# Kernel tuning notes

Hardware: AMD Instinct MI355X
Metric: run time of the kernel (lower is better)

The kernel has to match this reference:

```python
import jax, jax.numpy as jnp
import numpy as np

MIN_MAP = jnp.array([-3.602826, -3.602826, -3.602826], dtype=jnp.float32)

def _conv(x, w, stride, pad):
    return jax.lax.conv_general_dilated(x, w, (stride, stride), [(pad, pad), (pad, pad)],
                                        dimension_numbers=('NCHW', 'OIHW', 'NCHW'))

def _bn(x, g, b):
    # inference BatchNorm with running_mean=0, running_var=1 -> pure channel affine
    return x * g[None, :, None, None] + b[None, :, None, None]

def _maxpool2(x):
    return jax.lax.reduce_window(x, -jnp.inf, jax.lax.max, (1, 1, 2, 2), (1, 1, 2, 2), 'VALID')

def _rotations(angles):
    # angles: [N,3] (already multiplied by pi); matrix entries copied verbatim from the torch source
    c, s = jnp.cos(angles), jnp.sin(angles)
    z = jnp.zeros_like(c[:, 0]); o = jnp.ones_like(c[:, 0])
    Rx = jnp.stack([jnp.stack([o, z, z], -1),
                    jnp.stack([z, c[:, 0], s[:, 0]], -1),
                    jnp.stack([z, -s[:, 0], c[:, 0]], -1)], 1)
    Ry = jnp.stack([jnp.stack([c[:, 1], z, -s[:, 1]], -1),
                    jnp.stack([z, o, z], -1),
                    jnp.stack([s[:, 1], z, c[:, 1]], -1)], 1)
    Rz = jnp.stack([jnp.stack([c[:, 2], s[:, 2], z], -1),
                    jnp.stack([-s[:, 2], c[:, 2], z], -1),
                    jnp.stack([z, z, o], -1)], 1)
    return jnp.einsum('nij,njk,nkl->nil', Rx, Ry, Rz)  # [N,3,3]


def setup_inputs() -> dict:
    key = jax.random.key(0)
    ks = jax.random.split(key, 16)
    N, C, T, V, M = 32, 3, 224, 224, 2
    OC = 128
    def he(k, shape, fan_in):
        return jax.random.normal(k, shape, jnp.float32) * np.float32(np.sqrt(2.0 / fan_in))
    inp = {}
    inp['x'] = jax.random.normal(ks[0], (N, C, T, V, M), jnp.float32)
    inp['w1'] = he(ks[1], (OC, C, 5, 5), C * 25); inp['b1'] = jnp.zeros((OC,), jnp.float32)
    inp['g1'] = jnp.ones((OC,), jnp.float32); inp['be1'] = jnp.zeros((OC,), jnp.float32)
    inp['w2'] = he(ks[2], (OC, OC, 5, 5), OC * 25); inp['b2'] = jnp.zeros((OC,), jnp.float32)
    inp['g2'] = jnp.ones((OC,), jnp.float32); inp['be2'] = jnp.zeros((OC,), jnp.float32)
    feat = OC * (224 // 8) * (224 // 8)  # 100352
    inp['fw'] = jax.random.normal(ks[3], (6, feat), jnp.float32) * np.float32(np.sqrt(1.0 / feat))
    inp['fb'] = jnp.zeros((6,), jnp.float32)
    chans = [3, 64, 256, 512, 1024, 2048]  # surrogate ResNet-50-style /32 backbone
    for i in range(5):
        cin, cout = chans[i], chans[i + 1]
        inp['bw%d' % (i + 1)] = he(ks[4 + i], (cout, cin, 3, 3), cin * 9)
        inp['bg%d' % (i + 1)] = jnp.ones((cout,), jnp.float32)
        inp['bb%d' % (i + 1)] = jnp.zeros((cout,), jnp.float32)
    lin = 2048 * 7 * 7
    inp['lw'] = jax.random.normal(ks[10], (60, lin), jnp.float32) * np.float32(np.sqrt(1.0 / lin))
    inp['lb'] = jnp.zeros((60,), jnp.float32)
    return inp


def reference(x, w1, b1, g1, be1, w2, b2, g2, be2, fw, fb,
              bw1, bg1, bb1, bw2, bg2, bb2, bw3, bg3, bb3, bw4, bg4, bb4, bw5, bg5, bb5,
              lw, lb):
    N = x.shape[0]
    def person(xp):  # xp: [N,3,T,V]
        h = jax.nn.relu(_bn(_conv(xp, w1, 2, 2) + b1[None, :, None, None], g1, be1))
        h = jax.nn.relu(_bn(_conv(h, w2, 2, 2) + b2[None, :, None, None], g2, be2))
        h = _maxpool2(h)                       # [N,128,28,28]
        o = h.reshape(N, -1) @ fw.T + fb       # [N,6]
        # torch builds rotations from out[n,:3].item() -> constants w.r.t. autodiff
        R = _rotations(jax.lax.stop_gradient(o[:, :3]) * jnp.pi)
        xf = xp.reshape(N, 3, -1)
        rot = jnp.einsum('nij,njk->nik', R, xf)
        shift = jnp.einsum('nij,nj->ni', R, MIN_MAP[None, :] - o[:, 3:])
        bias = 255.0 * (shift - MIN_MAP[None, :]) / 8.812765
        z = (rot + bias[:, :, None]).reshape(xp.shape)
        for w, g, b in ((bw1, bg1, bb1), (bw2, bg2, bb2), (bw3, bg3, bb3),
                        (bw4, bg4, bb4), (bw5, bg5, bb5)):
            z = jax.nn.relu(_bn(_conv(z, w, 2, 1), g, b))
        return z  # [N,2048,7,7]
    out = jnp.maximum(person(x[..., 0]), person(x[..., 1]))
    return out.reshape(N, -1) @ lw.T + lb  # [N,60]
```

## Files before the change

kernel.cpp:

```cpp
#include <hip/hip_runtime.h>
#include <hip/hip_bf16.h>

typedef unsigned short u16;
typedef __attribute__((ext_vector_type(8))) short bf16x8;
typedef __attribute__((ext_vector_type(4))) float f32x4;
typedef __attribute__((ext_vector_type(8))) unsigned short u16x8;
typedef __attribute__((ext_vector_type(4))) unsigned short u16x4;

__device__ __forceinline__ u16 f2bf(float v) {
    __hip_bfloat16 b = __float2bfloat16(v);
    return *reinterpret_cast<u16*>(&b);
}
__device__ __forceinline__ float bf2f(u16 u) {
    __hip_bfloat16 b;
    *reinterpret_cast<u16*>(&b) = u;
    return __bfloat162float(b);
}

__device__ __forceinline__ void gl_lds16(const u16* g, u16* l) {
    __builtin_amdgcn_global_load_lds(
        (const __attribute__((address_space(1))) void*)g,
        (__attribute__((address_space(3))) void*)l, 16, 0, 0);
}

__global__ void repack_w32(const float* __restrict__ w, u16* __restrict__ wh,
                           int Cout, int Cin, int KK) {
    int i = blockIdx.x * blockDim.x + threadIdx.x;
    int tot = Cout * Cin * KK;
    if (i >= tot) return;
    int oc = i / (Cin * KK);
    int r = i - oc * (Cin * KK);
    int p = r / Cin, ic = r - p * Cin;
    wh[(size_t)oc * (Cin * KK) + (size_t)p * Cin + ic] =
        f2bf(w[((size_t)oc * Cin + ic) * KK + p]);
}
__global__ void repack_split2(const float* __restrict__ w, u16* __restrict__ Ap,
                              int Cout, int CinR, int CinP, int KK, int Ksteps) {
    int cols = Ksteps * 64;
    int idx = blockIdx.x * blockDim.x + threadIdx.x;
    int tot = Cout * cols;
    if (idx >= tot) return;
    int oc = idx / cols, c = idx - oc * cols;
    int t = c >> 6, r = c & 63, half = r >> 5, j = r & 31;
    int kk = t * 32 + j;
    int p = kk / CinP, ic = kk - p * CinP;
    float v = (p < KK && ic < CinR) ? w[((size_t)oc * CinR + ic) * KK + p] : 0.f;
    u16 h = f2bf(v);
    Ap[idx] = half ? f2bf(v - bf2f(h)) : h;
}
__global__ void repack_g4_2(const float* __restrict__ w, u16* __restrict__ Ap,
                            int Cout, int CinR, int KS, int Ksteps) {
    int cols = Ksteps * 64;
    int idx = blockIdx.x * blockDim.x + threadIdx.x;
    int tot = Cout * cols;
    if (idx >= tot) return;
    int oc = idx / cols, c = idx - oc * cols;
    int t = c >> 6, r = c & 63, half = r >> 5, j = r & 31;
    int pix = j >> 2, ch = j & 3;
    float v = (pix < KS && ch < CinR)
                  ? w[(((size_t)oc * CinR + ch) * KS + t) * KS + pix] : 0.f;
    u16 h = f2bf(v);
    Ap[idx] = half ? f2bf(v - bf2f(h)) : h;
}
__global__ void repack_g4(const float* __restrict__ w, u16* __restrict__ Ap,
                          int Cout, int CinR, int KS, int Kpp) {
    int idx = blockIdx.x * blockDim.x + threadIdx.x;
    int tot = Cout * Kpp;
    if (idx >= tot) return;
    int oc = idx / Kpp, kk = idx - oc * Kpp;
    int ky = kk >> 5, r = kk & 31;
    int pix = r >> 2, ch = r & 3;
    float v = (pix < KS && ch < CinR)
                  ? w[(((size_t)oc * CinR + ch) * KS + ky) * KS + pix] : 0.f;
    Ap[idx] = f2bf(v);
}

__global__ void extract_person4(const float* __restrict__ x,
                                u16* __restrict__ X4, int m, int total) {
    int idx = blockIdx.x * blockDim.x + threadIdx.x;
    if (idx >= total) return;
    int n = idx / 50176;
    int p = idx - n * 50176;
    int y = p / 224, xx = p - y * 224;
    u16 h[4];
    h[3] = 0;
#pragma unroll
    for (int c = 0; c < 3; ++c)
        h[c] = f2bf(x[(((size_t)(n * 3 + c)) * 50176 + p) * 2 + m]);
    size_t o = (((size_t)n * 228 + y + 2) * 232 + xx + 2) * 4;
    *reinterpret_cast<u16x4*>(&X4[o]) = *reinterpret_cast<u16x4*>(h);
}

__global__ void zero_u16(u16* __restrict__ b, size_t n8) {
    size_t i = (size_t)blockIdx.x * blockDim.x + threadIdx.x;
    if (i >= n8) return;
    u16x8 z = {0, 0, 0, 0, 0, 0, 0, 0};
    *reinterpret_cast<u16x8*>(&b[i * 8]) = z;
}
__global__ void zero_halo(u16* __restrict__ buf, int Nn, int Hp, int Wp, int C,
                          int P, int H, int W) {
    int idx = blockIdx.x * blockDim.x + threadIdx.x;
    int tot = Nn * Hp * Wp;
    if (idx >= tot) return;
    int x = idx % Wp, t = idx / Wp, y = t % Hp;
    if (y >= P && y < P + H && x >= P && x < P + W) return;
    u16* p = buf + (size_t)idx * C;
    u16x8 z = {0, 0, 0, 0, 0, 0, 0, 0};
    for (int c = 0; c < C; c += 8) *reinterpret_cast<u16x8*>(&p[c]) = z;
}

template <int BM, int CT, bool SPLIT, int MOUT>
__global__ __launch_bounds__(256) void gconv(
    const u16* __restrict__ A, const u16* __restrict__ B,
    const float* __restrict__ cbias, const float* __restrict__ gam,
    const float* __restrict__ bet,
    u16* __restrict__ outp, float* __restrict__ outf,
    int Nblk, int NHW, int Ksteps, int KSP,
    int Cin, int Hp_i, int Wp_i, int KS,
    int Wout, int HWout,
    int Cout, int Hp_o, int Wp_o, int P_o) {
    constexpr int WAVES_M = (BM == 128) ? 2 : 1;
    constexpr int WM = BM / WAVES_M;
    constexpr int WN = 128 / (4 / WAVES_M);
    constexpr int FM = WM / 16, FN = WN / 16;
    constexpr int ACOLS = SPLIT ? 64 : 32;
    constexpr int AR = (BM * ACOLS * 2) / 4096;

    __shared__ __align__(16) u16 Asb[2][BM * ACOLS];
    __shared__ __align__(16) u16 Bsb[2][128 * 32];

    const int tid = threadIdx.x;
    const int lane = tid & 63, wv = tid >> 6;

    const int nwg = gridDim.x, orig = blockIdx.x;
    const int qq = nwg >> 3, rr = nwg & 7, xcd = orig & 7;
    const int L = (xcd < rr ? xcd * (qq + 1) : rr * (qq + 1) + (xcd - rr) * qq) + (orig >> 3);
    const int gmK = nwg / Nblk;
    const int gm = gmK / KSP;
    const int bn = L / gmK;
    const int midK = L - bn * gmK;
    const int bm = midK % gm;
    const int kc = midK / gm;
    const int s0 = bn * 128, oc0 = bm * BM;

    const int nsteps = Ksteps;
    const int Arow = Ksteps * ACOLS;

    const u16* asrc[AR];
#pragma unroll
    for (int r = 0; r < AR; ++r) {
        int idx = r * 256 + tid;
        if constexpr (SPLIT) {
            int row = idx >> 3, slot = idx & 7;
            int c = slot ^ (row & 7);
            asrc[r] = A + (size_t)(oc0 + row) * Arow + c * 8;
        } else {
            int row = idx >> 2, slot = idx & 3;
            int q = slot ^ ((row >> 1) & 3);
            asrc[r] = A + (size_t)(oc0 + row) * Arow + q * 8;
        }
    }
    long brow[2];
#pragma unroll
    for (int r = 0; r < 2; ++r) {
        int idx = r * 256 + tid;
        int srow = idx >> 2;
        int q = (idx & 3) ^ ((idx >> 3) & 3);
        int s = s0 + srow;
        if (s > NHW - 1) s = NHW - 1;
        int n = s / HWout, pos = s - n * HWout;
        int oy = pos / Wout, ox = pos - oy * Wout;
        brow[r] = (((long)n * Hp_i + 2 * oy) * Wp_i + 2 * ox) * Cin + q * 8;
    }

    auto stage = [&](int buf, int t) {
        long ao = (long)t * ACOLS;
#pragma unroll
        for (int r = 0; r < AR; ++r)
            gl_lds16(asrc[r] + ao, &Asb[buf][(r * 256 + wv * 64) * 8]);
        long so;
        if constexpr (CT == 32) {
            int csn = Cin >> 5;
            int p = t / csn, cs = t - p * csn;
            int ky = p / KS, kx = p - ky * KS;
            so = (long)(ky * Wp_i + kx) * Cin + cs * 32;
        } else {
            so = (long)t * Wp_i * 4;
        }
#pragma unroll
        for (int r = 0; r < 2; ++r)
            gl_lds16(B + brow[r] + so, &Bsb[buf][(r * 256 + wv * 64) * 8]);
    };

    const int cl = lane & 15, oct = lane >> 4;
    const int octx = oct ^ ((cl >> 1) & 3);
    const int aslot = oct ^ (cl & 7);
    const int wm0 = (WAVES_M == 2) ? (wv & 1) * WM : 0;
    const int wn0 = (WAVES_M == 2) ? (wv >> 1) * WN : wv * WN;

    f32x4 acc[FM][FN] = {};

    const int cs_steps = nsteps / KSP;
    const int t0 = kc * cs_steps, t1 = t0 + cs_steps;

    stage(0, t0);
    __syncthreads();
    for (int t = t0; t < t1; ++t) {
        const int cur = (t - t0) & 1;
        if (t + 1 < t1) stage(cur ^ 1, t + 1);
        bf16x8 af[FM], bfr[FN];
#pragma unroll
        for (int mi = 0; mi < FM; ++mi) {
            if constexpr (SPLIT)
                af[mi] = *reinterpret_cast<const bf16x8*>(
                    &Asb[cur][(wm0 + mi * 16 + cl) * ACOLS + aslot * 8]);
            else
                af[mi] = *reinterpret_cast<const bf16x8*>(
                    &Asb[cur][(wm0 + mi * 16 + cl) * ACOLS + octx * 8]);
        }
#pragma unroll
        for (int ni = 0; ni < FN; ++ni)
            bfr[ni] = *reinterpret_cast<const bf16x8*>(
                &Bsb[cur][(wn0 + ni * 16 + cl) * 32 + octx * 8]);
#pragma unroll
        for (int mi = 0; mi < FM; ++mi)
#pragma unroll
            for (int ni = 0; ni < FN; ++ni)
                acc[mi][ni] = __builtin_amdgcn_mfma_f32_16x16x32_bf16(
                    af[mi], bfr[ni], acc[mi][ni], 0, 0, 0);
        if constexpr (SPLIT) {
            bf16x8 al[FM];
#pragma unroll
            for (int mi = 0; mi < FM; ++mi)
                al[mi] = *reinterpret_cast<const bf16x8*>(
                    &Asb[cur][(wm0 + mi * 16 + cl) * ACOLS + (aslot ^ 4) * 8]);
#pragma unroll
            for (int mi = 0; mi < FM; ++mi)
#pragma unroll
                for (int ni = 0; ni < FN; ++ni)
                    acc[mi][ni] = __builtin_amdgcn_mfma_f32_16x16x32_bf16(
                        al[mi], bfr[ni], acc[mi][ni], 0, 0, 0);
        }
        __syncthreads();
    }

#pragma unroll
    for (int ni = 0; ni < FN; ++ni) {
        int s = s0 + wn0 + ni * 16 + cl;
        if (s >= NHW) continue;
        int n = s / HWout, pos = s - n * HWout;
        int oy = pos / Wout, ox = pos - oy * Wout;
#pragma unroll
        for (int mi = 0; mi < FM; ++mi) {
            int oc = oc0 + wm0 + mi * 16 + oct * 4;
            if constexpr (MOUT == 3) {
                float* pf = outf + (size_t)kc * ((size_t)NHW * Cout);
#pragma unroll
                for (int r3 = 0; r3 < 4; ++r3)
                    pf[((size_t)n * Cout + oc + r3) * HWout + pos] = acc[mi][ni][r3];
            } else if constexpr (MOUT == 2) {
#pragma unroll
                for (int r3 = 0; r3 < 4; ++r3) {
                    float v = acc[mi][ni][r3];
                    if (cbias) v += cbias[oc + r3];
                    v = fmaf(v, gam[oc + r3], bet[oc + r3]);
                    v = fmaxf(v, 0.f);
                    outf[((size_t)n * Cout + oc + r3) * HWout + pos] = v;
                }
            } else {
                u16 hh[4];
#pragma unroll
                for (int r3 = 0; r3 < 4; ++r3) {
                    float v = acc[mi][ni][r3];
                    if (cbias) v += cbias[oc + r3];
                    v = fmaf(v, gam[oc + r3], bet[oc + r3]);
                    v = fmaxf(v, 0.f);
                    hh[r3] = f2bf(v);
                }
                size_t ob = (((size_t)n * Hp_o + oy + P_o) * Wp_o + ox + P_o) * Cout + oc;
                *reinterpret_cast<u16x4*>(&outp[ob]) = *reinterpret_cast<u16x4*>(hh);
            }
        }
    }
}

__global__ void ksum_nchw(const float* __restrict__ part, const float* __restrict__ gam,
                          const float* __restrict__ bet, float* __restrict__ out,
                          size_t tot, size_t str, int HWout, int Cout, int KSP,
                          int domax) {
    size_t i = (size_t)blockIdx.x * blockDim.x + threadIdx.x;
    if (i >= tot) return;
    float s = 0.f;
    for (int kc = 0; kc < KSP; ++kc) s += part[kc * str + i];
    int oc = (int)((i / HWout) % Cout);
    float v = fmaxf(fmaf(s, gam[oc], bet[oc]), 0.f);
    out[i] = domax ? fmaxf(out[i], v) : v;
}
__global__ void ksum_nhwc(const float* __restrict__ part, const float* __restrict__ gam,
                          const float* __restrict__ bet, u16* __restrict__ outp,
                          int NHW, int HWout, int Wout, int Cout,
                          int Hp, int Wp, int P, int KSP, size_t str) {
    int ocq = Cout >> 2;
    int idx = blockIdx.x * blockDim.x + threadIdx.x;
    if (idx >= NHW * ocq) return;
    int s = idx / ocq;
    int oc = (idx - s * ocq) * 4;
    int n = s / HWout, pos = s - n * HWout;
    int oy = pos / Wout, ox = pos - oy * Wout;
    u16 hh[4];
#pragma unroll
    for (int j = 0; j < 4; ++j) {
        float v = 0.f;
        for (int kc = 0; kc < KSP; ++kc)
            v += part[kc * str + ((size_t)n * Cout + oc + j) * HWout + pos];
        v = fmaxf(fmaf(v, gam[oc + j], bet[oc + j]), 0.f);
        hh[j] = f2bf(v);
    }
    size_t ob = (((size_t)n * Hp + oy + P) * Wp + ox + P) * Cout + oc;
    *reinterpret_cast<u16x4*>(&outp[ob]) = *reinterpret_cast<u16x4*>(hh);
}

__global__ void maxpool2(const float* __restrict__ in, float* __restrict__ out,
                         int NC, int H, int W) {
    int Ho = H >> 1, Wo = W >> 1;
    size_t idx = (size_t)blockIdx.x * blockDim.x + threadIdx.x;
    size_t total = (size_t)NC * Ho * Wo;
    if (idx >= total) return;
    int ox = idx % Wo;
    size_t t = idx / Wo;
    int oy = t % Ho;
    int nc = t / Ho;
    const float* p = in + ((size_t)nc * H + oy * 2) * W + ox * 2;
    out[idx] = fmaxf(fmaxf(p[0], p[1]), fmaxf(p[W], p[W + 1]));
}

__global__ __launch_bounds__(256) void lin_part(
    const float* __restrict__ X, const float* __restrict__ W,
    float* __restrict__ partial, int K, int Kc, int Ncols, int Nn) {
    int c = blockIdx.x / Nn;
    int n = blockIdx.x - c * Nn;
    int lane = threadIdx.x & 63, wv = threadIdx.x >> 6;
    const float4* x4 = reinterpret_cast<const float4*>(X + (size_t)n * K + (size_t)c * Kc);
    int K4 = Kc >> 2;
    for (int j = wv; j < Ncols; j += 4) {
        const float4* w4 =
            reinterpret_cast<const float4*>(W + (size_t)j * K + (size_t)c * Kc);
        float s = 0.f;
        for (int k = lane; k < K4; k += 64) {
            float4 a = x4[k], b = w4[k];
            s = fmaf(a.x, b.x, s);
            s = fmaf(a.y, b.y, s);
            s = fmaf(a.z, b.z, s);
            s = fmaf(a.w, b.w, s);
        }
#pragma unroll
        for (int off = 32; off > 0; off >>= 1) s += __shfl_down(s, off, 64);
        if (lane == 0) partial[((size_t)c * Nn + n) * 64 + j] = s;
    }
}

__global__ void lin_reduce(const float* __restrict__ partial,
                           const float* __restrict__ bias, float* __restrict__ out,
                           int Ncols, int Nn, int nchunks) {
    int t = blockIdx.x * blockDim.x + threadIdx.x;
    if (t >= Nn * Ncols) return;
    int n = t / Ncols, j = t - n * Ncols;
    float s = bias[j];
    for (int c = 0; c < nchunks; ++c) s += partial[((size_t)c * Nn + n) * 64 + j];
    out[t] = s;
}

__global__ void make_rot(const float* __restrict__ o6, float* __restrict__ R,
                         float* __restrict__ bv, int Nc) {
    int n = threadIdx.x;
    if (n >= Nc) return;
    const float PI = 3.14159265358979323846f;
    float a0 = o6[n * 6 + 0] * PI, a1 = o6[n * 6 + 1] * PI, a2 = o6[n * 6 + 2] * PI;
    float c0 = cosf(a0), c1 = cosf(a1), c2 = cosf(a2);
    float s0 = sinf(a0), s1 = sinf(a1), s2 = sinf(a2);
    float Rx[9] = {1, 0, 0, 0, c0, s0, 0, -s0, c0};
    float Ry[9] = {c1, 0, -s1, 0, 1, 0, s1, 0, c1};
    float Rz[9] = {c2, s2, 0, -s2, c2, 0, 0, 0, 1};
    float M[9], Rm[9];
#pragma unroll
    for (int i = 0; i < 3; ++i)
#pragma unroll
        for (int j = 0; j < 3; ++j) {
            float acc = 0.f;
#pragma unroll
            for (int k = 0; k < 3; ++k) acc = fmaf(Ry[i * 3 + k], Rz[k * 3 + j], acc);
            M[i * 3 + j] = acc;
        }
#pragma unroll
    for (int i = 0; i < 3; ++i)
#pragma unroll
        for (int j = 0; j < 3; ++j) {
            float acc = 0.f;
#pragma unroll
            for (int k = 0; k < 3; ++k) acc = fmaf(Rx[i * 3 + k], M[k * 3 + j], acc);
            Rm[i * 3 + j] = acc;
        }
    const float MINV = -3.602826f;
    float v0 = MINV - o6[n * 6 + 3];
    float v1 = MINV - o6[n * 6 + 4];
    float v2 = MINV - o6[n * 6 + 5];
#pragma unroll
    for (int i = 0; i < 3; ++i) {
        float sh = Rm[i * 3 + 0] * v0 + Rm[i * 3 + 1] * v1 + Rm[i * 3 + 2] * v2;
        bv[n * 3 + i] = 255.f * (sh - MINV) / 8.812765f;
        R[n * 9 + i * 3 + 0] = Rm[i * 3 + 0];
        R[n * 9 + i * 3 + 1] = Rm[i * 3 + 1];
        R[n * 9 + i * 3 + 2] = Rm[i * 3 + 2];
    }
}

__global__ void rot_apply5(const float* __restrict__ xc, const float* __restrict__ R,
                           const float* __restrict__ bv, u16* __restrict__ z,
                           int m, int total) {
    int idx = blockIdx.x * blockDim.x + threadIdx.x;
    if (idx >= total) return;
    int n = idx / 50176;
    int p = idx - n * 50176;
    int y = p / 224, xx = p - y * 224;
    float x0 = xc[(((size_t)(n * 3 + 0)) * 50176 + p) * 2 + m];
    float x1 = xc[(((size_t)(n * 3 + 1)) * 50176 + p) * 2 + m];
    float x2 = xc[(((size_t)(n * 3 + 2)) * 50176 + p) * 2 + m];
    u16 o[4];
#pragma unroll
    for (int i = 0; i < 3; ++i) {
        float v = fmaf(R[n * 9 + i * 3 + 0], x0,
                  fmaf(R[n * 9 + i * 3 + 1], x1,
                  fmaf(R[n * 9 + i * 3 + 2], x2, bv[n * 3 + i])));
        o[i] = f2bf(v);
    }
    o[3] = 0;
    size_t ob = (((size_t)n * 226 + y + 1) * 232 + xx + 1) * 4;
    *reinterpret_cast<u16x4*>(&z[ob]) = *reinterpret_cast<u16x4*>(o);
}

static inline int nblk(size_t total, int bs) { return (int)((total + bs - 1) / bs); }

extern "C" void kernel_launch(void* const* d_in, const int* in_sizes, int n_in,
                              void* d_out, int out_size, void* d_ws, size_t ws_size,
                              hipStream_t stream) {
    const float* x   = (const float*)d_in[0];
    const float* w1  = (const float*)d_in[1];
    const float* b1  = (const float*)d_in[2];
    const float* g1  = (const float*)d_in[3];
    const float* be1 = (const float*)d_in[4];
    const float* w2  = (const float*)d_in[5];
    const float* b2  = (const float*)d_in[6];
    const float* g2  = (const float*)d_in[7];
    const float* be2 = (const float*)d_in[8];
    const float* fw  = (const float*)d_in[9];
    const float* fb  = (const float*)d_in[10];
    const float* bw[5], *bg[5], *bb[5];
    for (int i = 0; i < 5; ++i) {
        bw[i] = (const float*)d_in[11 + 3 * i];
        bg[i] = (const float*)d_in[12 + 3 * i];
        bb[i] = (const float*)d_in[13 + 3 * i];
    }
    const float* lw = (const float*)d_in[26];
    const float* lb = (const float*)d_in[27];
    float* out = (float*)d_out;

    const int N = 32;
    const int BS = 256;
    const size_t S_Pp = 100352;

    const size_t E_X4 = (size_t)228 * 232 * 4;
    const size_t E_Z  = (size_t)226 * 232 * 4;
    const size_t E_B1 = (size_t)116 * 116 * 128;
    const size_t E_Zb2 = (size_t)114 * 114 * 64;
    const size_t E_Zb3 = (size_t)58 * 58 * 256;
    const size_t E_Zb4 = (size_t)30 * 30 * 512;
    const size_t E_Zb5 = (size_t)16 * 16 * 1024;

    const size_t slotC_B = E_Zb2 * 2;
    const size_t per_sample_B = E_X4 * 2 + E_Z * 2 +
                                E_B1 * 2 + slotC_B + S_Pp * 4;
    const size_t apack_u16 = (size_t)128 * 320 + (size_t)128 * 6400 + (size_t)64 * 96 +
                             (size_t)256 * 576 + (size_t)512 * 2304 +
                             (size_t)1024 * 4608 + (size_t)2048 * 9216;
    const size_t fixed_B = (size_t)N * S_Pp * 4 + 131072 * 4 + 8192 + apack_u16 * 2 + 4096;

    int Nc = N;
    while (Nc > 1 && (size_t)Nc * per_sample_B + fixed_B > ws_size) Nc >>= 1;

    char* cur = (char*)d_ws;
    auto alf = [&](size_t n) { float* p = (float*)cur; cur += ((n + 3) & ~(size_t)3) * 4; return p; };
    auto alu = [&](size_t n) { u16* p = (u16*)cur; cur += ((n + 7) & ~(size_t)7) * 2; return p; };

    float* PM = alf((size_t)N * S_Pp);
    float* O6 = alf(256);
    float* Rm = alf(384);
    float* BV = alf(384);
    float* LP = alf(131072);
    u16* Ap1 = alu((size_t)128 * 320);
    u16* Ap2 = alu((size_t)128 * 6400);
    u16* Ab1 = alu((size_t)64 * 96);
    u16* Ab2 = alu((size_t)256 * 576);
    u16* Ab3 = alu((size_t)512 * 2304);
    u16* Ab4 = alu((size_t)1024 * 4608);
    u16* Ab5 = alu((size_t)2048 * 9216);

    u16* X4p   = alu((size_t)Nc * E_X4);
    u16* Z16p  = alu((size_t)Nc * E_Z);
    u16* B1p   = alu((size_t)Nc * E_B1);
    u16* Zb3   = B1p;
    u16* Zb4   = Zb3 + (size_t)Nc * E_Zb3;
    u16* Zb5   = Zb4 + (size_t)Nc * E_Zb4;
    u16* SLOTC = alu((size_t)Nc * slotC_B / 2);
    float* C2f = (float*)SLOTC;
    u16* Zb2   = SLOTC;
    float* PartF = (float*)SLOTC;
    float* Pp  = alf((size_t)Nc * S_Pp);

    repack_g4_2<<<nblk((size_t)128 * 320, BS), BS, 0, stream>>>(w1, Ap1, 128, 3, 5, 5);
    repack_split2<<<nblk((size_t)128 * 6400, BS), BS, 0, stream>>>(w2, Ap2, 128, 128, 128, 25, 100);
    repack_g4<<<nblk((size_t)64 * 96, BS), BS, 0, stream>>>(bw[0], Ab1, 64, 3, 3, 96);
    repack_w32<<<nblk((size_t)256 * 576, BS), BS, 0, stream>>>(bw[1], Ab2, 256, 64, 9);
    repack_w32<<<nblk((size_t)512 * 2304, BS), BS, 0, stream>>>(bw[2], Ab3, 512, 256, 9);
    repack_w32<<<nblk((size_t)1024 * 4608, BS), BS, 0, stream>>>(bw[3], Ab4, 1024, 512, 9);
    repack_w32<<<nblk((size_t)2048 * 9216, BS), BS, 0, stream>>>(bw[4], Ab5, 2048, 1024, 9);

    zero_u16<<<nblk((size_t)Nc * E_X4 / 8, BS), BS, 0, stream>>>(X4p, (size_t)Nc * E_X4 / 8);
    zero_u16<<<nblk((size_t)Nc * E_Z / 8, BS), BS, 0, stream>>>(Z16p, (size_t)Nc * E_Z / 8);

    const int NHW1 = Nc * 12544;
    const int Nb1 = (NHW1 + 127) / 128;
    const int NHW2 = Nc * 3136;
    const int Nb2 = (NHW2 + 127) / 128;
    const int NHW3 = Nc * 784;
    const int Nb3 = (NHW3 + 127) / 128;
    const int NHW4 = Nc * 196;
    const int Nb4 = (NHW4 + 127) / 128;
    const int NHW5 = Nc * 49;
    const int Nb5 = (NHW5 + 127) / 128;
    const size_t str4 = (size_t)NHW4 * 1024;
    const size_t str5 = (size_t)NHW5 * 2048;

    for (int m = 0; m < 2; ++m) {
        for (int c0 = 0; c0 < N; c0 += Nc) {
            const float* xc = x + (size_t)c0 * 150528 * 2;
            int nNP = Nc * 50176;
            extract_person4<<<nblk(nNP, BS), BS, 0, stream>>>(xc, X4p, m, nNP);

            zero_halo<<<nblk((size_t)Nc * 116 * 116, BS), BS, 0, stream>>>(B1p, Nc, 116, 116, 128, 2, 112, 112);

            gconv<128, 4, true, 0><<<Nb1, 256, 0, stream>>>(
                Ap1, X4p, b1, g1, be1, B1p, nullptr,
                Nb1, NHW1, 5, 1, 4, 228, 232, 5, 112, 12544, 128, 116, 116, 2);
            gconv<128, 32, true, 2><<<Nb2, 256, 0, stream>>>(
                Ap2, B1p, b2, g2, be2, nullptr, C2f,
                Nb2, NHW2, 100, 1, 128, 116, 116, 5, 56, 3136, 128, 0, 0, 0);

            size_t nP = (size_t)Nc * S_Pp;
            maxpool2<<<nblk(nP, BS), BS, 0, stream>>>(C2f, Pp, Nc * 128, 56, 56);
            lin_part<<<64 * Nc, 256, 0, stream>>>(Pp, fw, LP, 100352, 1568, 6, Nc);
            lin_reduce<<<nblk(Nc * 6, 64), 64, 0, stream>>>(LP, fb, O6, 6, Nc, 64);
            make_rot<<<1, 64, 0, stream>>>(O6, Rm, BV, Nc);
            rot_apply5<<<nblk(nNP, BS), BS, 0, stream>>>(xc, Rm, BV, Z16p, m, nNP);

            zero_halo<<<nblk((size_t)Nc * 114 * 114, BS), BS, 0, stream>>>(Zb2, Nc, 114, 114, 64, 1, 112, 112);
            zero_halo<<<nblk((size_t)Nc * 58 * 58, BS), BS, 0, stream>>>(Zb3, Nc, 58, 58, 256, 1, 56, 56);
            zero_halo<<<nblk((size_t)Nc * 30 * 30, BS), BS, 0, stream>>>(Zb4, Nc, 30, 30, 512, 1, 28, 28);
            zero_halo<<<nblk((size_t)Nc * 16 * 16, BS), BS, 0, stream>>>(Zb5, Nc, 16, 16, 1024, 1, 14, 14);

            gconv<64, 4, false, 0><<<Nb1, 256, 0, stream>>>(
                Ab1, Z16p, nullptr, bg[0], bb[0], Zb2, nullptr,
                Nb1, NHW1, 3, 1, 4, 226, 232, 3, 112, 12544, 64, 114, 114, 1);
            gconv<128, 32, false, 0><<<2 * Nb2, 256, 0, stream>>>(
                Ab2, Zb2, nullptr, bg[1], bb[1], Zb3, nullptr,
                Nb2, NHW2, 18, 1, 64, 114, 114, 3, 56, 3136, 256, 58, 58, 1);
            gconv<128, 32, false, 0><<<4 * Nb3, 256, 0, stream>>>(
                Ab3, Zb3, nullptr, bg[2], bb[2], Zb4, nullptr,
                Nb3, NHW3, 72, 1, 256, 58, 58, 3, 28, 784, 512, 30, 30, 1);
            gconv<128, 32, false, 3><<<8 * 2 * Nb4, 256, 0, stream>>>(
                Ab4, Zb4, nullptr, nullptr, nullptr, nullptr, PartF,
                Nb4, NHW4, 144, 2, 512, 30, 30, 3, 14, 196, 1024, 0, 0, 0);
            ksum_nhwc<<<nblk((size_t)NHW4 * 256, BS), BS, 0, stream>>>(
                PartF, bg[3], bb[3], Zb5, NHW4, 196, 14, 1024, 16, 16, 1, 2, str4);
            gconv<128, 32, false, 3><<<16 * 4 * Nb5, 256, 0, stream>>>(
                Ab5, Zb5, nullptr, nullptr, nullptr, nullptr, PartF,
                Nb5, NHW5, 288, 4, 1024, 16, 16, 3, 7, 49, 2048, 0, 0, 0);
            float* PMc = PM + (size_t)c0 * S_Pp;
            ksum_nchw<<<nblk((size_t)NHW5 * 2048, BS), BS, 0, stream>>>(
                PartF, bg[4], bb[4], PMc, (size_t)NHW5 * 2048, str5, 49, 2048, 4, m);
        }
    }

    lin_part<<<64 * N, 256, 0, stream>>>(PM, lw, LP, 100352, 1568, 60, N);
    lin_reduce<<<nblk(N * 60, 64), 64, 0, stream>>>(LP, lb, out, 60, N, 64);
}
```

Baseline: 2.060 ms.

## Add split-K to conv2, backbone layer 3, and deeper layers when workspace allows

```diff
diff --git a/kernel.cpp b/kernel.cpp
--- a/kernel.cpp
+++ b/kernel.cpp
@@ -318,6 +318,30 @@
     }
     size_t ob = (((size_t)n * Hp + oy + P) * Wp + ox + P) * Cout + oc;
     *reinterpret_cast<u16x4*>(&outp[ob]) = *reinterpret_cast<u16x4*>(hh);
+}
+
+__global__ void maxpool_ks(const float* __restrict__ part, const float* __restrict__ cbias,
+                           const float* __restrict__ gam, const float* __restrict__ bet,
+                           float* __restrict__ out, int NC, int KSP, size_t str) {
+    int idx = blockIdx.x * blockDim.x + threadIdx.x;
+    if (idx >= NC * 784) return;
+    int nc = idx / 784;
+    int r = idx - nc * 784;
+    int oy = r / 28, ox = r - oy * 28;
+    int oc = nc & 127;
+    float cb = cbias[oc], g = gam[oc], be = bet[oc];
+    float m = -1e30f;
+#pragma unroll
+    for (int dy = 0; dy < 2; ++dy)
+#pragma unroll
+        for (int dx = 0; dx < 2; ++dx) {
+            size_t off = (size_t)nc * 3136 + (2 * oy + dy) * 56 + 2 * ox + dx;
+            float s = 0.f;
+            for (int kc = 0; kc < KSP; ++kc) s += part[kc * str + off];
+            s = fmaxf(fmaf(s + cb, g, be), 0.f);
+            m = fmaxf(m, s);
+        }
+    out[idx] = m;
 }
 
 __global__ void maxpool2(const float* __restrict__ in, float* __restrict__ out,
@@ -476,16 +500,18 @@
     const size_t E_Zb4 = (size_t)30 * 30 * 512;
     const size_t E_Zb5 = (size_t)16 * 16 * 1024;
 
-    const size_t slotC_B = E_Zb2 * 2;
-    const size_t per_sample_B = E_X4 * 2 + E_Z * 2 +
-                                E_B1 * 2 + slotC_B + S_Pp * 4;
+    const size_t slotC_small = E_Zb2 * 2;
+    const size_t slotC_big = (size_t)2 * 3136 * 128 * 4;
+    const size_t base_B = E_X4 * 2 + E_Z * 2 + E_B1 * 2 + S_Pp * 4;
     const size_t apack_u16 = (size_t)128 * 320 + (size_t)128 * 6400 + (size_t)64 * 96 +
                              (size_t)256 * 576 + (size_t)512 * 2304 +
                              (size_t)1024 * 4608 + (size_t)2048 * 9216;
     const size_t fixed_B = (size_t)N * S_Pp * 4 + 131072 * 4 + 8192 + apack_u16 * 2 + 4096;
 
     int Nc = N;
-    while (Nc > 1 && (size_t)Nc * per_sample_B + fixed_B > ws_size) Nc >>= 1;
+    while (Nc > 1 && (size_t)Nc * (base_B + slotC_small) + fixed_B > ws_size) Nc >>= 1;
+    const bool big = ((size_t)Nc * (base_B + slotC_big) + fixed_B) <= ws_size;
+    const size_t slotC_B = big ? slotC_big : slotC_small;
 
     char* cur = (char*)d_ws;
     auto alf = [&](size_t n) { float* p = (float*)cur; cur += ((n + 3) & ~(size_t)3) * 4; return p; };
@@ -537,8 +563,12 @@
     const int Nb4 = (NHW4 + 127) / 128;
     const int NHW5 = Nc * 49;
     const int Nb5 = (NHW5 + 127) / 128;
+    const size_t str2 = (size_t)NHW2 * 128;
+    const size_t str3 = (size_t)NHW3 * 512;
     const size_t str4 = (size_t)NHW4 * 1024;
     const size_t str5 = (size_t)NHW5 * 2048;
+    const int KSP4 = big ? 4 : 2;
+    const int KSP5 = big ? 8 : 4;
 
     for (int m = 0; m < 2; ++m) {
         for (int c0 = 0; c0 < N; c0 += Nc) {
@@ -551,12 +581,20 @@
             gconv<128, 4, true, 0><<<Nb1, 256, 0, stream>>>(
                 Ap1, X4p, b1, g1, be1, B1p, nullptr,
                 Nb1, NHW1, 5, 1, 4, 228, 232, 5, 112, 12544, 128, 116, 116, 2);
-            gconv<128, 32, true, 2><<<Nb2, 256, 0, stream>>>(
-                Ap2, B1p, b2, g2, be2, nullptr, C2f,
-                Nb2, NHW2, 100, 1, 128, 116, 116, 5, 56, 3136, 128, 0, 0, 0);
-
-            size_t nP = (size_t)Nc * S_Pp;
-            maxpool2<<<nblk(nP, BS), BS, 0, stream>>>(C2f, Pp, Nc * 128, 56, 56);
+
+            if (big) {
+                gconv<128, 32, true, 3><<<2 * Nb2, 256, 0, stream>>>(
+                    Ap2, B1p, nullptr, nullptr, nullptr, nullptr, PartF,
+                    Nb2, NHW2, 100, 2, 128, 116, 116, 5, 56, 3136, 128, 0, 0, 0);
+                maxpool_ks<<<nblk((size_t)Nc * S_Pp, BS), BS, 0, stream>>>(
+                    PartF, b2, g2, be2, Pp, Nc * 128, 2, str2);
+            } else {
+                gconv<128, 32, true, 2><<<Nb2, 256, 0, stream>>>(
+                    Ap2, B1p, b2, g2, be2, nullptr, C2f,
+                    Nb2, NHW2, 100, 1, 128, 116, 116, 5, 56, 3136, 128, 0, 0, 0);
+                maxpool2<<<nblk((size_t)Nc * S_Pp, BS), BS, 0, stream>>>(C2f, Pp, Nc * 128, 56, 56);
+            }
+
             lin_part<<<64 * Nc, 256, 0, stream>>>(Pp, fw, LP, 100352, 1568, 6, Nc);
             lin_reduce<<<nblk(Nc * 6, 64), 64, 0, stream>>>(LP, fb, O6, 6, Nc, 64);
             make_rot<<<1, 64, 0, stream>>>(O6, Rm, BV, Nc);
@@ -573,20 +611,28 @@
             gconv<128, 32, false, 0><<<2 * Nb2, 256, 0, stream>>>(
                 Ab2, Zb2, nullptr, bg[1], bb[1], Zb3, nullptr,
                 Nb2, NHW2, 18, 1, 64, 114, 114, 3, 56, 3136, 256, 58, 58, 1);
-            gconv<128, 32, false, 0><<<4 * Nb3, 256, 0, stream>>>(
-                Ab3, Zb3, nullptr, bg[2], bb[2], Zb4, nullptr,
-                Nb3, NHW3, 72, 1, 256, 58, 58, 3, 28, 784, 512, 30, 30, 1);
-            gconv<128, 32, false, 3><<<8 * 2 * Nb4, 256, 0, stream>>>(
+            if (big) {
+                gconv<128, 32, false, 3><<<4 * 2 * Nb3, 256, 0, stream>>>(
+                    Ab3, Zb3, nullptr, nullptr, nullptr, nullptr, PartF,
+                    Nb3, NHW3, 72, 2, 256, 58, 58, 3, 28, 784, 512, 30, 30, 1);
+                ksum_nhwc<<<nblk((size_t)NHW3 * 128, BS), BS, 0, stream>>>(
+                    PartF, bg[2], bb[2], Zb4, NHW3, 784, 28, 512, 30, 30, 1, 2, str3);
+            } else {
+                gconv<128, 32, false, 0><<<4 * Nb3, 256, 0, stream>>>(
+                    Ab3, Zb3, nullptr, bg[2], bb[2], Zb4, nullptr,
+                    Nb3, NHW3, 72, 1, 256, 58, 58, 3, 28, 784, 512, 30, 30, 1);
+            }
+            gconv<128, 32, false, 3><<<8 * KSP4 * Nb4, 256, 0, stream>>>(
                 Ab4, Zb4, nullptr, nullptr, nullptr, nullptr, PartF,
-                Nb4, NHW4, 144, 2, 512, 30, 30, 3, 14, 196, 1024, 0, 0, 0);
+                Nb4, NHW4, 144, KSP4, 512, 30, 30, 3, 14, 196, 1024, 0, 0, 0);
             ksum_nhwc<<<nblk((size_t)NHW4 * 256, BS), BS, 0, stream>>>(
-                PartF, bg[3], bb[3], Zb5, NHW4, 196, 14, 1024, 16, 16, 1, 2, str4);
-            gconv<128, 32, false, 3><<<16 * 4 * Nb5, 256, 0, stream>>>(
+                PartF, bg[3], bb[3], Zb5, NHW4, 196, 14, 1024, 16, 16, 1, KSP4, str4);
+            gconv<128, 32, false, 3><<<16 * KSP5 * Nb5, 256, 0, stream>>>(
                 Ab5, Zb5, nullptr, nullptr, nullptr, nullptr, PartF,
-                Nb5, NHW5, 288, 4, 1024, 16, 16, 3, 7, 49, 2048, 0, 0, 0);
+                Nb5, NHW5, 288, KSP5, 1024, 16, 16, 3, 7, 49, 2048, 0, 0, 0);
             float* PMc = PM + (size_t)c0 * S_Pp;
             ksum_nchw<<<nblk((size_t)NHW5 * 2048, BS), BS, 0, stream>>>(
-                PartF, bg[4], bb[4], PMc, (size_t)NHW5 * 2048, str5, 49, 2048, 4, m);
+                PartF, bg[4], bb[4], PMc, (size_t)NHW5 * 2048, str5, 49, 2048, KSP5, m);
         }
     }
 
```

Result: no change. 2.061 ms (+0.1%).
